# Optimization experiments

Measured on AMD Instinct MI355X. Metric: run time of the kernel, lower is better.

The kernel has to match this reference:

```python
import jax, jax.numpy as jnp
import numpy as np

K3 = 27            # kernel_size**3
PAIRS_PER_K = 131072  # pairs per kernel offset (equal-size segments)
N_VOX = 262144     # active voxels (stride-1, same grid: N_in == N_out)
C_IN = 32
C_OUT = 32


def setup_inputs() -> dict:
    key = jax.random.key(0)
    k1, k2, k3, k4 = jax.random.split(key, 4)
    M = K3 * PAIRS_PER_K
    in_feature = jax.random.normal(k1, (N_VOX, C_IN), dtype=jnp.float32)
    kernel = jax.random.normal(k2, (K3, C_IN, C_OUT), dtype=jnp.float32) * (1.0 / np.sqrt(C_IN * K3))
    bias = jax.random.normal(k3, (C_OUT,), dtype=jnp.float32) * 0.01
    # nbmap[:, 0] = input voxel index, nbmap[:, 1] = output voxel index,
    # sorted by kernel offset (offset k owns rows [k*P, (k+1)*P)).
    nbmap = jax.random.randint(k4, (M, 2), 0, N_VOX, dtype=jnp.int32)
    nbsizes = jnp.full((K3,), PAIRS_PER_K, dtype=jnp.int32)
    return {"in_feature": in_feature, "kernel": kernel, "bias": bias,
            "nbmap": nbmap, "nbsizes": nbsizes}


def reference(in_feature, kernel, bias, nbmap, nbsizes):
    """Gather -> per-offset GEMM -> scatter-add, matching
    ext.conv.sparse_convolution for a stride-1 non-transposed conv where
    nbmap rows are grouped by kernel offset with equal segment sizes."""
    k3, c_in, c_out = kernel.shape
    m = nbmap.shape[0]
    p = m // k3  # pairs per offset (static)
    n_out = in_feature.shape[0]  # same grid, stride 1
    # gather input features for every (input, output) pair  [M, C_in]
    gathered = in_feature[nbmap[:, 0]]
    # batched GEMM: one [P, C_in] x [C_in, C_out] per kernel offset
    contrib = jnp.einsum('kpi,kio->kpo', gathered.reshape(k3, p, c_in), kernel)
    contrib = contrib.reshape(m, c_out)
    # scatter-add contributions into output voxels
    out = jax.ops.segment_sum(contrib, nbmap[:, 1], num_segments=n_out)
    return out + bias
```

## Files before the change

kernel.cpp:

```cpp
#include <hip/hip_runtime.h>
#include <hip/hip_bf16.h>


#define N_VOX    262144
#define LOG2_NV  18
#define C_CH     32
#define K3       27
#define LOG2_PPK 17
#define BLOCK    256
#define FLAG_FIN 0x40000000
#define ECAP     4096
#define PLPAD    36
#define FRAGN    (K3 * 2 * 64)
#define NF16     (N_VOX * 4)

typedef __attribute__((ext_vector_type(8))) short bf16x8;
typedef __attribute__((ext_vector_type(4))) float f32x4;
typedef unsigned long long ull;

#define PMASK   0x3FFFFFull
#define EMPTY2(w) (((w) >> 58) == 0x3Full)

__device__ __forceinline__ unsigned short f2bf(float f) {
  union { __hip_bfloat16 h; unsigned short u; } cv;
  cv.h = __float2bfloat16(f);
  return cv.u;
}

__global__ __launch_bounds__(BLOCK) void setup_kernel(
    int4* __restrict__ clrT, long nt4, int4* __restrict__ clrC, long nc4,
    const float* __restrict__ in_feature, unsigned short* __restrict__ feat16,
    int use16, const float* __restrict__ kernel_w,
    unsigned short* __restrict__ Bf) {
  long idx = (long)blockIdx.x * BLOCK + threadIdx.x;
  if (idx < nt4) {
    clrT[idx] = make_int4(-1, -1, -1, -1);
    return;
  }
  idx -= nt4;
  if (idx < nc4) {
    clrC[idx] = make_int4(0, 0, 0, 0);
    return;
  }
  idx -= nc4;
  if (use16) {
    if (idx < NF16) {
      const float4* src = (const float4*)in_feature + (idx << 1);
      float4 f0 = src[0], f1 = src[1];
      union { unsigned short u[8]; uint4 v; } pk;
      pk.u[0] = f2bf(f0.x); pk.u[1] = f2bf(f0.y);
      pk.u[2] = f2bf(f0.z); pk.u[3] = f2bf(f0.w);
      pk.u[4] = f2bf(f1.x); pk.u[5] = f2bf(f1.y);
      pk.u[6] = f2bf(f1.z); pk.u[7] = f2bf(f1.w);
      ((uint4*)feat16)[idx] = pk.v;
      return;
    }
    idx -= NF16;
  }
  if (idx < FRAGN) {
    int wid = (int)idx;
    int lane = wid & 63;
    int kc = wid >> 6;
    int k = kc >> 1, t = kc & 1;
    int i0 = (lane >> 4) * 8;
    int c = t * 16 + (lane & 15);
    union { unsigned short u[8]; uint4 v; } pk;
#pragma unroll
    for (int j = 0; j < 8; ++j)
      pk.u[j] = f2bf(kernel_w[(k << 10) + (i0 + j) * C_CH + c]);
    ((uint4*)Bf)[wid] = pk.v;
  }
}

__global__ __launch_bounds__(BLOCK) void passA_packed(
    const int4* __restrict__ nbmap2, ull* __restrict__ T64, int Mq) {
  int q = blockIdx.x * BLOCK + threadIdx.x;
  if (q >= Mq) return;
  int4 na = nbmap2[q * 2];
  int4 nb = nbmap2[q * 2 + 1];
  int p0 = q << 2, p1 = p0 | 1, p2 = p0 | 2, p3 = p0 | 3;
  const ull EM = 0x3Full << 58;
  T64[((long)(p0 >> LOG2_PPK) << LOG2_NV) + na.y] =
      (ull)p0 | ((ull)na.x << 22) | EM;
  T64[((long)(p1 >> LOG2_PPK) << LOG2_NV) + na.w] =
      (ull)p1 | ((ull)na.z << 22) | EM;
  T64[((long)(p2 >> LOG2_PPK) << LOG2_NV) + nb.y] =
      (ull)p2 | ((ull)nb.x << 22) | EM;
  T64[((long)(p3 >> LOG2_PPK) << LOG2_NV) + nb.w] =
      (ull)p3 | ((ull)nb.z << 22) | EM;
}

__device__ __forceinline__ void ovf_push(
    int vox, int k, int in, int* __restrict__ ovf_cnt, int* __restrict__ ovf,
    int S2, int* __restrict__ ecnt, int2* __restrict__ elist) {
  int pos = atomicAdd(&ovf_cnt[vox], 1);
  if (pos < S2) {
    ovf[(pos << LOG2_NV) + vox] = (k << LOG2_NV) | in;
  } else {
    int ep = atomicAdd(ecnt, 1);
    if (ep < ECAP) elist[ep] = make_int2(vox, (k << LOG2_NV) | in);
  }
}

__device__ __forceinline__ void resolve_packed(
    int p, int vox, int in, ull w, ull* __restrict__ T64, long idx,
    int* __restrict__ ovf_cnt, int* __restrict__ ovf, int S2,
    int* __restrict__ ecnt, int2* __restrict__ elist) {
  if ((w & PMASK) == (ull)p) return;
  ull cur = w;
  for (;;) {
    if (!EMPTY2(cur)) break;
    ull nw = (cur & ((1ull << 40) - 1)) | ((ull)in << 40);
    ull old = atomicCAS(&T64[idx], cur, nw);
    if (old == cur) return;
    cur = old;
  }
  ovf_push(vox, p >> LOG2_PPK, in, ovf_cnt, ovf, S2, ecnt, elist);
}

__global__ __launch_bounds__(BLOCK) void passB_packed(
    const int4* __restrict__ nbmap2, ull* __restrict__ T64,
    int* __restrict__ ovf_cnt, int* __restrict__ ovf, int S2,
    int* __restrict__ ecnt, int2* __restrict__ elist, int Mq) {
  int q = blockIdx.x * BLOCK + threadIdx.x;
  if (q >= Mq) return;
  int4 na = nbmap2[q * 2];
  int4 nb = nbmap2[q * 2 + 1];
  int p0 = q << 2, p1 = p0 | 1, p2 = p0 | 2, p3 = p0 | 3;
  long i0 = ((long)(p0 >> LOG2_PPK) << LOG2_NV) + na.y;
  long i1 = ((long)(p1 >> LOG2_PPK) << LOG2_NV) + na.w;
  long i2 = ((long)(p2 >> LOG2_PPK) << LOG2_NV) + nb.y;
  long i3 = ((long)(p3 >> LOG2_PPK) << LOG2_NV) + nb.w;
  ull w0 = T64[i0];
  ull w1 = T64[i1];
  ull w2 = T64[i2];
  ull w3 = T64[i3];
  resolve_packed(p0, na.y, na.x, w0, T64, i0, ovf_cnt, ovf, S2, ecnt, elist);
  resolve_packed(p1, na.w, na.z, w1, T64, i1, ovf_cnt, ovf, S2, ecnt, elist);
  resolve_packed(p2, nb.y, nb.x, w2, T64, i2, ovf_cnt, ovf, S2, ecnt, elist);
  resolve_packed(p3, nb.w, nb.z, w3, T64, i3, ovf_cnt, ovf, S2, ecnt, elist);
}

__global__ __launch_bounds__(BLOCK) void passA_legacy(
    const int2* __restrict__ nbmap, int* __restrict__ T, int M) {
  int p = blockIdx.x * BLOCK + threadIdx.x;
  if (p >= M) return;
  int2 nb = nbmap[p];
  T[((p >> LOG2_PPK) << LOG2_NV) + nb.y] = p;
}

__global__ __launch_bounds__(BLOCK) void passB_legacy(
    const int2* __restrict__ nbmap, int* __restrict__ T,
    int* __restrict__ ovf_cnt, int* __restrict__ ovf, int S2,
    int* __restrict__ ecnt, int2* __restrict__ elist, int M) {
  int p = blockIdx.x * BLOCK + threadIdx.x;
  if (p >= M) return;
  int2 nb = nbmap[p];
  int idx = ((p >> LOG2_PPK) << LOG2_NV) + nb.y;
  if (T[idx] == p) {
    T[idx] = FLAG_FIN | nb.x;
  } else {
    ovf_push(nb.y, p >> LOG2_PPK, nb.x, ovf_cnt, ovf, S2, ecnt, elist);
  }
}

template <int PACKED, int F16>
__global__ __launch_bounds__(BLOCK, 4) void gather_splitk_kernel(
    const float* __restrict__ in_feature,
    const unsigned short* __restrict__ feat16,
    const float* __restrict__ kernel_w,
    const float* __restrict__ bias,
    const void* __restrict__ Tv,
    const int* __restrict__ ovf_cnt,
    const int* __restrict__ ovf,
    const unsigned short* __restrict__ Bf,
    float* __restrict__ out, int S2) {
  __shared__ float plane[4][16][PLPAD];
  __shared__ int flatE[256];
  __shared__ int scnt[16];

  const int tid = threadIdx.x;
  const int w = tid >> 6;
  const int lane = tid & 63;
  const int r16 = lane & 15;
  const int quad = lane >> 4;
  const int vb = blockIdx.x << 4;

  const int er = tid & 15;
  const int ej = tid >> 4;
  int eval = 0;
  if (ej < S2)
    eval = ovf[(ej << LOG2_NV) + vb + er];
  if (tid < 16) {
    int c = ovf_cnt[vb + tid];
    scnt[tid] = c < S2 ? c : S2;
  }
  const int kb = w * 7;
  const int kn = (w == 3) ? 6 : 7;
  const int v = vb + r16;

  ull wv[7];
  if (PACKED) {
    const ull* T64 = (const ull*)Tv;
#pragma unroll
    for (int d = 0; d < 7; ++d)
      wv[d] = (d < kn) ? T64[((long)(kb + d) << LOG2_NV) + v] : ~0ull;
  } else {
    const int* T = (const int*)Tv;
#pragma unroll
    for (int d = 0; d < 7; ++d) {
      int t = (d < kn) ? T[((kb + d) << LOG2_NV) + v] : -1;
      wv[d] = (t >= 0) ? (((ull)(t & 0x3FFFF) << 22) | (0x3Full << 58))
                       : ~0ull;
    }
  }
  __syncthreads();

  int myb = 0, tot = 0;
#pragma unroll
  for (int q = 0; q < 16; ++q) {
    int cq = scnt[q];
    if (q < er) myb += cq;
    tot += cq;
  }
  if (ej < scnt[er])
    flatE[myb + ej] = (er << 24) | eval;
  __syncthreads();

  bf16x8 R0[7], R1[7];
#pragma unroll
  for (int d = 0; d < 7; ++d) {
    bool val1 = (wv[d] & PMASK) != PMASK;
    int in = val1 ? (int)((wv[d] >> 22) & 0x3FFFF) : 0;
    bf16x8 a;
    if (F16) {
      a = *reinterpret_cast<const bf16x8*>(feat16 + (in << 5) + (quad << 3));
    } else {
      const float4* ap = (const float4*)(in_feature + (in << 5) + (quad << 3));
      float4 f0 = ap[0], f1 = ap[1];
      a[0] = (short)f2bf(f0.x); a[1] = (short)f2bf(f0.y);
      a[2] = (short)f2bf(f0.z); a[3] = (short)f2bf(f0.w);
      a[4] = (short)f2bf(f1.x); a[5] = (short)f2bf(f1.y);
      a[6] = (short)f2bf(f1.z); a[7] = (short)f2bf(f1.w);
    }
    if (!val1) a = (bf16x8)0;
    R0[d] = a;
  }
  if (PACKED) {
#pragma unroll
    for (int d = 0; d < 7; ++d) {
      bool val2 = !EMPTY2(wv[d]);
      int in = val2 ? (int)((wv[d] >> 40) & 0x3FFFF) : 0;
      bf16x8 a;
      if (F16) {
        a = *reinterpret_cast<const bf16x8*>(feat16 + (in << 5) + (quad << 3));
      } else {
        const float4* ap =
            (const float4*)(in_feature + (in << 5) + (quad << 3));
        float4 f0 = ap[0], f1 = ap[1];
        a[0] = (short)f2bf(f0.x); a[1] = (short)f2bf(f0.y);
        a[2] = (short)f2bf(f0.z); a[3] = (short)f2bf(f0.w);
        a[4] = (short)f2bf(f1.x); a[5] = (short)f2bf(f1.y);
        a[6] = (short)f2bf(f1.z); a[7] = (short)f2bf(f1.w);
      }
      if (!val2) a = (bf16x8)0;
      R1[d] = a;
    }
  }

  f32x4 acc0 = {0.f, 0.f, 0.f, 0.f};
  f32x4 acc1 = {0.f, 0.f, 0.f, 0.f};
  const uint4* bfp = (const uint4*)Bf;
#pragma unroll
  for (int d = 0; d < 7; ++d) {
    if (d < kn) {
      int k = kb + d;
      uint4 h0 = bfp[(k * 2 + 0) * 64 + lane];
      uint4 h1 = bfp[(k * 2 + 1) * 64 + lane];
      acc0 = __builtin_amdgcn_mfma_f32_16x16x32_bf16(
          R0[d], *reinterpret_cast<const bf16x8*>(&h0), acc0, 0, 0, 0);
      acc1 = __builtin_amdgcn_mfma_f32_16x16x32_bf16(
          R0[d], *reinterpret_cast<const bf16x8*>(&h1), acc1, 0, 0, 0);
    }
  }
  if (PACKED) {
#pragma unroll
    for (int d = 0; d < 7; ++d) {
      if (d < kn) {
        int k = kb + d;
        uint4 h0 = bfp[(k * 2 + 0) * 64 + lane];
        uint4 h1 = bfp[(k * 2 + 1) * 64 + lane];
        acc0 = __builtin_amdgcn_mfma_f32_16x16x32_bf16(
            R1[d], *reinterpret_cast<const bf16x8*>(&h0), acc0, 0, 0, 0);
        acc1 = __builtin_amdgcn_mfma_f32_16x16x32_bf16(
            R1[d], *reinterpret_cast<const bf16x8*>(&h1), acc1, 0, 0, 0);
      }
    }
  }

#pragma unroll
  for (int reg = 0; reg < 4; ++reg) {
    int row = quad * 4 + reg;
    plane[w][row][r16] = acc0[reg];
    plane[w][row][16 + r16] = acc1[reg];
  }

  const int c32 = lane & 31, h = lane >> 5;
  int i = w;
  int e_cur = 0;
  float4 p0, p1, p2, p3;
  if (i < tot) {
    e_cur = flatE[i];
    const float4* ar =
        (const float4*)(in_feature + ((e_cur & 0x3FFFF) << 5) + (h << 4));
    p0 = ar[0]; p1 = ar[1]; p2 = ar[2]; p3 = ar[3];
  }
  while (i < tot) {
    const int e = e_cur;
    float4 q0 = p0, q1 = p1, q2 = p2, q3 = p3;
    const int inext = i + 4;
    if (inext < tot) {
      e_cur = flatE[inext];
      const float4* ar =
          (const float4*)(in_feature + ((e_cur & 0x3FFFF) << 5) + (h << 4));
      p0 = ar[0]; p1 = ar[1]; p2 = ar[2]; p3 = ar[3];
    }
    const int k2 = (e >> LOG2_NV) & 31;
    const int rr = (e >> 24) & 15;
    const float* wcol = kernel_w + (k2 << 10) + (h << 4) * C_CH + c32;
    float psum = 0.f;
    psum = fmaf(q0.x, wcol[0 * C_CH], psum);
    psum = fmaf(q0.y, wcol[1 * C_CH], psum);
    psum = fmaf(q0.z, wcol[2 * C_CH], psum);
    psum = fmaf(q0.w, wcol[3 * C_CH], psum);
    psum = fmaf(q1.x, wcol[4 * C_CH], psum);
    psum = fmaf(q1.y, wcol[5 * C_CH], psum);
    psum = fmaf(q1.z, wcol[6 * C_CH], psum);
    psum = fmaf(q1.w, wcol[7 * C_CH], psum);
    psum = fmaf(q2.x, wcol[8 * C_CH], psum);
    psum = fmaf(q2.y, wcol[9 * C_CH], psum);
    psum = fmaf(q2.z, wcol[10 * C_CH], psum);
    psum = fmaf(q2.w, wcol[11 * C_CH], psum);
    psum = fmaf(q3.x, wcol[12 * C_CH], psum);
    psum = fmaf(q3.y, wcol[13 * C_CH], psum);
    psum = fmaf(q3.z, wcol[14 * C_CH], psum);
    psum = fmaf(q3.w, wcol[15 * C_CH], psum);
    psum += __shfl_xor(psum, 32);
    if (h == 0) plane[w][rr][c32] += psum;
    i = inext;
  }

  __syncthreads();
  const int mr = tid >> 4;
  const int mc = (tid & 15) << 1;
  float s0 = plane[0][mr][mc] + plane[1][mr][mc] + plane[2][mr][mc] +
             plane[3][mr][mc] + bias[mc];
  float s1 = plane[0][mr][mc + 1] + plane[1][mr][mc + 1] +
             plane[2][mr][mc + 1] + plane[3][mr][mc + 1] + bias[mc + 1];
  float2 o; o.x = s0; o.y = s1;
  *(float2*)(out + ((vb + mr) << 5) + mc) = o;
}

__global__ __launch_bounds__(BLOCK) void emergency_kernel(
    const float* __restrict__ in_feature, const float* __restrict__ kernel_w,
    const int* __restrict__ ecnt, const int2* __restrict__ elist,
    float* __restrict__ out) {
  int e = blockIdx.x * BLOCK + threadIdx.x;
  int n = *ecnt;
  if (n > ECAP) n = ECAP;
  if (e >= n) return;
  int2 ent = elist[e];
  int v = ent.x, k = ent.y >> LOG2_NV, in = ent.y & 0x3FFFF;
  float a[C_CH];
  const float4* ar = (const float4*)(in_feature + (in << 5));
#pragma unroll
  for (int q = 0; q < 8; ++q) ((float4*)a)[q] = ar[q];
  for (int c = 0; c < C_CH; ++c) {
    float s = 0.f;
#pragma unroll
    for (int i = 0; i < C_CH; ++i)
      s = fmaf(a[i], kernel_w[(k << 10) + i * C_CH + c], s);
    atomicAdd(&out[v * C_CH + c], s);
  }
}

__global__ __launch_bounds__(BLOCK) void init_bias_kernel(
    float* __restrict__ out, const float* __restrict__ bias, int n4) {
  int idx = blockIdx.x * blockDim.x + threadIdx.x;
  if (idx >= n4) return;
  ((float4*)out)[idx] = ((const float4*)bias)[idx & 7];
}

__global__ __launch_bounds__(BLOCK) void scatter_conv_kernel(
    const float* __restrict__ in_feature, const float* __restrict__ kernel_w,
    const int* __restrict__ nbmap, float* __restrict__ out) {
  const int k = blockIdx.x >> 9;
  const int pair = blockIdx.x * BLOCK + threadIdx.x;
  const float* __restrict__ Wk = kernel_w + k * (C_CH * C_CH);
  const int2 nb = ((const int2*)nbmap)[pair];
  const float4* __restrict__ inrow =
      (const float4*)(in_feature + (long)nb.x * C_CH);
  float a[C_CH];
#pragma unroll
  for (int j = 0; j < 8; ++j) ((float4*)a)[j] = inrow[j];
  float acc[C_CH];
#pragma unroll
  for (int c = 0; c < C_CH; ++c) acc[c] = 0.0f;
#pragma unroll
  for (int i = 0; i < C_CH; ++i) {
    const float av = a[i];
#pragma unroll
    for (int c = 0; c < C_CH; ++c)
      acc[c] = fmaf(av, Wk[i * C_CH + c], acc[c]);
  }
  float* __restrict__ orow = out + (long)nb.y * C_CH;
#pragma unroll
  for (int c = 0; c < C_CH; ++c) atomicAdd(orow + c, acc[c]);
}

extern "C" void kernel_launch(void* const* d_in, const int* in_sizes, int n_in,
                              void* d_out, int out_size, void* d_ws,
                              size_t ws_size, hipStream_t stream) {
  const float* in_feature = (const float*)d_in[0];
  const float* kernel_w   = (const float*)d_in[1];
  const float* bias       = (const float*)d_in[2];
  const int*   nbmap      = (const int*)d_in[3];
  float* out = (float*)d_out;
  const int M = in_sizes[3] / 2;
  const int Mq = M / 4;

  const long FIXED = 64 + 2 * ECAP + 13824;
  long ws_ints = (long)(ws_size / 4);
  long planes = (ws_ints - FIXED) / N_VOX;
  int packed = 0, use16 = 0;
  long s2c;
  if (planes >= 75) {
    packed = 1; use16 = 1;
    s2c = planes - 71;
    if (s2c > 7) s2c = 7;
  } else if (planes >= 59) {
    packed = 1;
    s2c = planes - 55;
    if (s2c > 7) s2c = 7;
  } else {
    s2c = planes - 28;
    if (s2c > 15) s2c = 15;
  }
  int S2 = (int)s2c;

  if (!packed && S2 < 4) {
    const int n4 = out_size / 4;
    init_bias_kernel<<<(n4 + BLOCK - 1) / BLOCK, BLOCK, 0, stream>>>(out, bias,
                                                                     n4);
    scatter_conv_kernel<<<M / BLOCK, BLOCK, 0, stream>>>(in_feature, kernel_w,
                                                         nbmap, out);
    return;
  }

  const long planesT = packed ? 2L * K3 : (long)K3;
  int* Tbase    = (int*)d_ws;
  int* ovf_cnt  = Tbase + planesT * N_VOX;
  int* ecnt     = ovf_cnt + N_VOX;
  int2* elist   = (int2*)(ecnt + 64);
  unsigned short* Bf = (unsigned short*)(ecnt + 64 + 2 * ECAP);
  int* ovf      = ((int*)Bf) + 13824;
  unsigned short* feat16 = (unsigned short*)(ovf + (long)S2 * N_VOX);

  const long nt4 = planesT * N_VOX / 4;
  const long nc4 = (N_VOX + 64) / 4;
  const long total = nt4 + nc4 + (use16 ? (long)NF16 : 0) + FRAGN;
  const long sblocks = (total + BLOCK - 1) / BLOCK;
  setup_kernel<<<(int)sblocks, BLOCK, 0, stream>>>(
      (int4*)Tbase, nt4, (int4*)ovf_cnt, nc4, in_feature, feat16, use16,
      kernel_w, Bf);

  if (packed) {
    passA_packed<<<(Mq + BLOCK - 1) / BLOCK, BLOCK, 0, stream>>>(
        (const int4*)nbmap, (ull*)Tbase, Mq);
    passB_packed<<<(Mq + BLOCK - 1) / BLOCK, BLOCK, 0, stream>>>(
        (const int4*)nbmap, (ull*)Tbase, ovf_cnt, ovf, S2, ecnt, elist, Mq);
    if (use16)
      gather_splitk_kernel<1, 1><<<N_VOX / 16, BLOCK, 0, stream>>>(
          in_feature, feat16, kernel_w, bias, (const void*)Tbase, ovf_cnt,
          ovf, Bf, out, S2);
    else
      gather_splitk_kernel<1, 0><<<N_VOX / 16, BLOCK, 0, stream>>>(
          in_feature, feat16, kernel_w, bias, (const void*)Tbase, ovf_cnt,
          ovf, Bf, out, S2);
  } else {
    passA_legacy<<<(M + BLOCK - 1) / BLOCK, BLOCK, 0, stream>>>(
        (const int2*)nbmap, Tbase, M);
    passB_legacy<<<(M + BLOCK - 1) / BLOCK, BLOCK, 0, stream>>>(
        (const int2*)nbmap, Tbase, ovf_cnt, ovf, S2, ecnt, elist, M);
    gather_splitk_kernel<0, 0><<<N_VOX / 16, BLOCK, 0, stream>>>(
        in_feature, feat16, kernel_w, bias, (const void*)Tbase, ovf_cnt, ovf,
        Bf, out, S2);
  }
  emergency_kernel<<<ECAP / BLOCK, BLOCK, 0, stream>>>(in_feature, kernel_w,
                                                       ecnt, elist, out);
}
```

Before: 362.0 us.

## Replace two-pass write/resolve table build with single atomicMax claim pass

The two kernels that built the packed 64-bit per-(offset, voxel) table, a plain-store pass followed by a CAS resolve pass, are merged into one kernel. Each pair now does a 64-bit atomicMax with a key that puts the pair index in the high bits, then resolves losers into a second-slot CAS or the overflow list. The table word layout is redesigned (zero means empty, bit 0 flags the second input), and the setup fill value and the gather kernel's decoding change to match. This removes one full pass over nbmap and the table, at the cost of atomic RMW traffic on every insert.

```diff
diff --git a/kernel.cpp b/kernel.cpp
--- a/kernel.cpp
+++ b/kernel.cpp
@@ -18,9 +18,6 @@
 typedef __attribute__((ext_vector_type(4))) float f32x4;
 typedef unsigned long long ull;
 
-#define PMASK   0x3FFFFFull
-#define EMPTY2(w) (((w) >> 58) == 0x3Full)
-
 __device__ __forceinline__ unsigned short f2bf(float f) {
   union { __hip_bfloat16 h; unsigned short u; } cv;
   cv.h = __float2bfloat16(f);
@@ -28,13 +25,13 @@
 }
 
 __global__ __launch_bounds__(BLOCK) void setup_kernel(
-    int4* __restrict__ clrT, long nt4, int4* __restrict__ clrC, long nc4,
-    const float* __restrict__ in_feature, unsigned short* __restrict__ feat16,
-    int use16, const float* __restrict__ kernel_w,
-    unsigned short* __restrict__ Bf) {
+    int4* __restrict__ clrT, long nt4, int cv, int4* __restrict__ clrC,
+    long nc4, const float* __restrict__ in_feature,
+    unsigned short* __restrict__ feat16, int use16,
+    const float* __restrict__ kernel_w, unsigned short* __restrict__ Bf) {
   long idx = (long)blockIdx.x * BLOCK + threadIdx.x;
   if (idx < nt4) {
-    clrT[idx] = make_int4(-1, -1, -1, -1);
+    clrT[idx] = make_int4(cv, cv, cv, cv);
     return;
   }
   idx -= nt4;
@@ -72,24 +69,6 @@
   }
 }
 
-__global__ __launch_bounds__(BLOCK) void passA_packed(
-    const int4* __restrict__ nbmap2, ull* __restrict__ T64, int Mq) {
-  int q = blockIdx.x * BLOCK + threadIdx.x;
-  if (q >= Mq) return;
-  int4 na = nbmap2[q * 2];
-  int4 nb = nbmap2[q * 2 + 1];
-  int p0 = q << 2, p1 = p0 | 1, p2 = p0 | 2, p3 = p0 | 3;
-  const ull EM = 0x3Full << 58;
-  T64[((long)(p0 >> LOG2_PPK) << LOG2_NV) + na.y] =
-      (ull)p0 | ((ull)na.x << 22) | EM;
-  T64[((long)(p1 >> LOG2_PPK) << LOG2_NV) + na.w] =
-      (ull)p1 | ((ull)na.z << 22) | EM;
-  T64[((long)(p2 >> LOG2_PPK) << LOG2_NV) + nb.y] =
-      (ull)p2 | ((ull)nb.x << 22) | EM;
-  T64[((long)(p3 >> LOG2_PPK) << LOG2_NV) + nb.w] =
-      (ull)p3 | ((ull)nb.z << 22) | EM;
-}
-
 __device__ __forceinline__ void ovf_push(
     int vox, int k, int in, int* __restrict__ ovf_cnt, int* __restrict__ ovf,
     int S2, int* __restrict__ ecnt, int2* __restrict__ elist) {
@@ -102,23 +81,40 @@
   }
 }
 
-__device__ __forceinline__ void resolve_packed(
-    int p, int vox, int in, ull w, ull* __restrict__ T64, long idx,
+__device__ __forceinline__ void in2_insert(
+    ull* __restrict__ T64, long idx, ull cur, int vox, int k, int in,
     int* __restrict__ ovf_cnt, int* __restrict__ ovf, int S2,
     int* __restrict__ ecnt, int2* __restrict__ elist) {
-  if ((w & PMASK) == (ull)p) return;
-  ull cur = w;
   for (;;) {
-    if (!EMPTY2(cur)) break;
-    ull nw = (cur & ((1ull << 40) - 1)) | ((ull)in << 40);
-    ull old = atomicCAS(&T64[idx], cur, nw);
-    if (old == cur) return;
-    cur = old;
-  }
-  ovf_push(vox, p >> LOG2_PPK, in, ovf_cnt, ovf, S2, ecnt, elist);
-}
-
-__global__ __launch_bounds__(BLOCK) void passB_packed(
+    if (cur & 1ull) {
+      ovf_push(vox, k, in, ovf_cnt, ovf, S2, ecnt, elist);
+      return;
+    }
+    ull nw = cur | ((ull)in << 6) | 1ull;
+    ull got = atomicCAS(&T64[idx], cur, nw);
+    if (got == cur) return;
+    cur = got;
+  }
+}
+
+__device__ __forceinline__ void resolve_max(
+    ull* __restrict__ T64, long idx, ull myw, ull old, int vox, int k, int in,
+    int* __restrict__ ovf_cnt, int* __restrict__ ovf, int S2,
+    int* __restrict__ ecnt, int2* __restrict__ elist) {
+  if (old == 0) return;
+  if (old < myw) {
+    int in1p = (int)((old >> 24) & 0x3FFFF);
+    if (old & 1ull) {
+      int in2p = (int)((old >> 6) & 0x3FFFF);
+      ovf_push(vox, k, in2p, ovf_cnt, ovf, S2, ecnt, elist);
+    }
+    in2_insert(T64, idx, myw, vox, k, in1p, ovf_cnt, ovf, S2, ecnt, elist);
+  } else {
+    in2_insert(T64, idx, old, vox, k, in, ovf_cnt, ovf, S2, ecnt, elist);
+  }
+}
+
+__global__ __launch_bounds__(BLOCK) void claim_max_kernel(
     const int4* __restrict__ nbmap2, ull* __restrict__ T64,
     int* __restrict__ ovf_cnt, int* __restrict__ ovf, int S2,
     int* __restrict__ ecnt, int2* __restrict__ elist, int Mq) {
@@ -127,18 +123,24 @@
   int4 na = nbmap2[q * 2];
   int4 nb = nbmap2[q * 2 + 1];
   int p0 = q << 2, p1 = p0 | 1, p2 = p0 | 2, p3 = p0 | 3;
-  long i0 = ((long)(p0 >> LOG2_PPK) << LOG2_NV) + na.y;
-  long i1 = ((long)(p1 >> LOG2_PPK) << LOG2_NV) + na.w;
-  long i2 = ((long)(p2 >> LOG2_PPK) << LOG2_NV) + nb.y;
-  long i3 = ((long)(p3 >> LOG2_PPK) << LOG2_NV) + nb.w;
-  ull w0 = T64[i0];
-  ull w1 = T64[i1];
-  ull w2 = T64[i2];
-  ull w3 = T64[i3];
-  resolve_packed(p0, na.y, na.x, w0, T64, i0, ovf_cnt, ovf, S2, ecnt, elist);
-  resolve_packed(p1, na.w, na.z, w1, T64, i1, ovf_cnt, ovf, S2, ecnt, elist);
-  resolve_packed(p2, nb.y, nb.x, w2, T64, i2, ovf_cnt, ovf, S2, ecnt, elist);
-  resolve_packed(p3, nb.w, nb.z, w3, T64, i3, ovf_cnt, ovf, S2, ecnt, elist);
+  int k0 = p0 >> LOG2_PPK, k1 = p1 >> LOG2_PPK;
+  int k2 = p2 >> LOG2_PPK, k3 = p3 >> LOG2_PPK;
+  long i0 = ((long)k0 << LOG2_NV) + na.y;
+  long i1 = ((long)k1 << LOG2_NV) + na.w;
+  long i2 = ((long)k2 << LOG2_NV) + nb.y;
+  long i3 = ((long)k3 << LOG2_NV) + nb.w;
+  ull w0 = ((ull)(p0 + 1) << 42) | ((ull)na.x << 24);
+  ull w1 = ((ull)(p1 + 1) << 42) | ((ull)na.z << 24);
+  ull w2 = ((ull)(p2 + 1) << 42) | ((ull)nb.x << 24);
+  ull w3 = ((ull)(p3 + 1) << 42) | ((ull)nb.z << 24);
+  ull o0 = atomicMax(&T64[i0], w0);
+  ull o1 = atomicMax(&T64[i1], w1);
+  ull o2 = atomicMax(&T64[i2], w2);
+  ull o3 = atomicMax(&T64[i3], w3);
+  resolve_max(T64, i0, w0, o0, na.y, k0, na.x, ovf_cnt, ovf, S2, ecnt, elist);
+  resolve_max(T64, i1, w1, o1, na.w, k1, na.z, ovf_cnt, ovf, S2, ecnt, elist);
+  resolve_max(T64, i2, w2, o2, nb.y, k2, nb.x, ovf_cnt, ovf, S2, ecnt, elist);
+  resolve_max(T64, i3, w3, o3, nb.w, k3, nb.z, ovf_cnt, ovf, S2, ecnt, elist);
 }
 
 __global__ __launch_bounds__(BLOCK) void passA_legacy(
@@ -204,14 +206,13 @@
     const ull* T64 = (const ull*)Tv;
 #pragma unroll
     for (int d = 0; d < 7; ++d)
-      wv[d] = (d < kn) ? T64[((long)(kb + d) << LOG2_NV) + v] : ~0ull;
+      wv[d] = (d < kn) ? T64[((long)(kb + d) << LOG2_NV) + v] : 0ull;
   } else {
     const int* T = (const int*)Tv;
 #pragma unroll
     for (int d = 0; d < 7; ++d) {
       int t = (d < kn) ? T[((kb + d) << LOG2_NV) + v] : -1;
-      wv[d] = (t >= 0) ? (((ull)(t & 0x3FFFF) << 22) | (0x3Full << 58))
-                       : ~0ull;
+      wv[d] = (t >= 0) ? ((1ull << 42) | ((ull)(t & 0x3FFFF) << 24)) : 0ull;
     }
   }
   __syncthreads();
@@ -230,8 +231,8 @@
   bf16x8 R0[7], R1[7];
 #pragma unroll
   for (int d = 0; d < 7; ++d) {
-    bool val1 = (wv[d] & PMASK) != PMASK;
-    int in = val1 ? (int)((wv[d] >> 22) & 0x3FFFF) : 0;
+    bool val1 = (wv[d] >> 42) != 0;
+    int in = val1 ? (int)((wv[d] >> 24) & 0x3FFFF) : 0;
     bf16x8 a;
     if (F16) {
       a = *reinterpret_cast<const bf16x8*>(feat16 + (in << 5) + (quad << 3));
@@ -249,8 +250,8 @@
   if (PACKED) {
 #pragma unroll
     for (int d = 0; d < 7; ++d) {
-      bool val2 = !EMPTY2(wv[d]);
-      int in = val2 ? (int)((wv[d] >> 40) & 0x3FFFF) : 0;
+      bool val2 = (wv[d] & 1ull) != 0;
+      int in = val2 ? (int)((wv[d] >> 6) & 0x3FFFF) : 0;
       bf16x8 a;
       if (F16) {
         a = *reinterpret_cast<const bf16x8*>(feat16 + (in << 5) + (quad << 3));
@@ -471,13 +472,11 @@
   const long total = nt4 + nc4 + (use16 ? (long)NF16 : 0) + FRAGN;
   const long sblocks = (total + BLOCK - 1) / BLOCK;
   setup_kernel<<<(int)sblocks, BLOCK, 0, stream>>>(
-      (int4*)Tbase, nt4, (int4*)ovf_cnt, nc4, in_feature, feat16, use16,
-      kernel_w, Bf);
+      (int4*)Tbase, nt4, packed ? 0 : -1, (int4*)ovf_cnt, nc4, in_feature,
+      feat16, use16, kernel_w, Bf);
 
   if (packed) {
-    passA_packed<<<(Mq + BLOCK - 1) / BLOCK, BLOCK, 0, stream>>>(
-        (const int4*)nbmap, (ull*)Tbase, Mq);
-    passB_packed<<<(Mq + BLOCK - 1) / BLOCK, BLOCK, 0, stream>>>(
+    claim_max_kernel<<<(Mq + BLOCK - 1) / BLOCK, BLOCK, 0, stream>>>(
         (const int4*)nbmap, (ull*)Tbase, ovf_cnt, ovf, S2, ecnt, elist, Mq);
     if (use16)
       gather_splitk_kernel<1, 1><<<N_VOX / 16, BLOCK, 0, stream>>>(
```

Measured after the change: 416.2 us. +15.0%, slower.

## Fuse setup and claim passes into one cooperative kernel with grid syncs

Applied to the files above, without the earlier changes.

Replaces the separate setup, passA and passB launches with a single cooperative kernel of fixed grid size that clears tables, converts features and weights, writes claims, then resolves collisions, separated by grid-wide barriers. The emergency overflow handling moves into the tail of the gather kernel, where each block scans the overflow list for its own voxels. This removes several kernel launches and the inter-kernel gaps, but it depends on cooperative launch, hardcodes the problem size, and makes every gather block scan the overflow list.

```diff
diff --git a/kernel.cpp b/kernel.cpp
--- a/kernel.cpp
+++ b/kernel.cpp
@@ -1,5 +1,8 @@
 #include <hip/hip_runtime.h>
 #include <hip/hip_bf16.h>
+#include <hip/hip_cooperative_groups.h>
+
+namespace cg = cooperative_groups;
 
 
 #define N_VOX    262144
@@ -13,6 +16,7 @@
 #define PLPAD    36
 #define FRAGN    (K3 * 2 * 64)
 #define NF16     (N_VOX * 4)
+#define CBLOCKS  864
 
 typedef __attribute__((ext_vector_type(8))) short bf16x8;
 typedef __attribute__((ext_vector_type(4))) float f32x4;
@@ -27,14 +31,131 @@
   return cv.u;
 }
 
-__global__ __launch_bounds__(BLOCK) void setup_kernel(
-    int4* __restrict__ clrT, long nt4, int4* __restrict__ clrC, long nc4,
+__device__ __forceinline__ void ovf_push(
+    int vox, int k, int in, int* __restrict__ ovf_cnt, int* __restrict__ ovf,
+    int S2, int* __restrict__ ecnt, int2* __restrict__ elist) {
+  int pos = atomicAdd(&ovf_cnt[vox], 1);
+  if (pos < S2) {
+    ovf[(pos << LOG2_NV) + vox] = (k << LOG2_NV) | in;
+  } else {
+    int ep = atomicAdd(ecnt, 1);
+    if (ep < ECAP) elist[ep] = make_int2(vox, (k << LOG2_NV) | in);
+  }
+}
+
+__device__ __forceinline__ void resolve_packed(
+    int p, int vox, int in, ull w, ull* __restrict__ T64, long idx,
+    int* __restrict__ ovf_cnt, int* __restrict__ ovf, int S2,
+    int* __restrict__ ecnt, int2* __restrict__ elist) {
+  if ((w & PMASK) == (ull)p) return;
+  ull cur = w;
+  for (;;) {
+    if (!EMPTY2(cur)) break;
+    ull nw = (cur & ((1ull << 40) - 1)) | ((ull)in << 40);
+    ull old = atomicCAS(&T64[idx], cur, nw);
+    if (old == cur) return;
+    cur = old;
+  }
+  ovf_push(vox, p >> LOG2_PPK, in, ovf_cnt, ovf, S2, ecnt, elist);
+}
+
+__device__ __forceinline__ void feat16_item(
+    const float* __restrict__ in_feature, unsigned short* __restrict__ feat16,
+    long idx) {
+  const float4* src = (const float4*)in_feature + (idx << 1);
+  float4 f0 = src[0], f1 = src[1];
+  union { unsigned short u[8]; uint4 v; } pk;
+  pk.u[0] = f2bf(f0.x); pk.u[1] = f2bf(f0.y);
+  pk.u[2] = f2bf(f0.z); pk.u[3] = f2bf(f0.w);
+  pk.u[4] = f2bf(f1.x); pk.u[5] = f2bf(f1.y);
+  pk.u[6] = f2bf(f1.z); pk.u[7] = f2bf(f1.w);
+  ((uint4*)feat16)[idx] = pk.v;
+}
+
+__device__ __forceinline__ void bf_item(
+    const float* __restrict__ kernel_w, unsigned short* __restrict__ Bf,
+    int wid) {
+  int lane = wid & 63;
+  int kc = wid >> 6;
+  int k = kc >> 1, t = kc & 1;
+  int i0 = (lane >> 4) * 8;
+  int c = t * 16 + (lane & 15);
+  union { unsigned short u[8]; uint4 v; } pk;
+#pragma unroll
+  for (int j = 0; j < 8; ++j)
+    pk.u[j] = f2bf(kernel_w[(k << 10) + (i0 + j) * C_CH + c]);
+  ((uint4*)Bf)[wid] = pk.v;
+}
+
+__global__ __launch_bounds__(BLOCK, 4) void fused_setup_claim(
+    const int4* __restrict__ nbmap2, ull* __restrict__ T64,
+    int* __restrict__ ovf_cnt, int* __restrict__ ovf, int S2,
+    int* __restrict__ ecnt, int2* __restrict__ elist,
     const float* __restrict__ in_feature, unsigned short* __restrict__ feat16,
     int use16, const float* __restrict__ kernel_w,
     unsigned short* __restrict__ Bf) {
+  const int t = blockIdx.x * BLOCK + threadIdx.x;
+  const long NT = (long)CBLOCKS * BLOCK;
+
+  {
+    int4* clrT = (int4*)T64;
+    const int4 m1 = make_int4(-1, -1, -1, -1);
+#pragma unroll
+    for (int i = 0; i < 16; ++i) clrT[(long)i * NT + t] = m1;
+    if (t < (N_VOX + 64) / 4) ((int4*)ovf_cnt)[t] = make_int4(0, 0, 0, 0);
+    if (use16)
+      for (long i = t; i < NF16; i += NT) feat16_item(in_feature, feat16, i);
+    if (t < FRAGN) bf_item(kernel_w, Bf, t);
+  }
+  cg::this_grid().sync();
+
+  {
+    const ull EM = 0x3Full << 58;
+#pragma unroll
+    for (int j = 0; j < 8; ++j) {
+      int4 A = nbmap2[(long)8 * t + j];
+      int pa = (t << 4) | (j << 1);
+      int pb = pa | 1;
+      T64[((long)(pa >> LOG2_PPK) << LOG2_NV) + A.y] =
+          (ull)pa | ((ull)A.x << 22) | EM;
+      T64[((long)(pb >> LOG2_PPK) << LOG2_NV) + A.w] =
+          (ull)pb | ((ull)A.z << 22) | EM;
+    }
+  }
+  cg::this_grid().sync();
+
+#pragma unroll 1
+  for (int g = 3; g >= 0; --g) {
+    int4 A = nbmap2[(long)8 * t + 2 * g];
+    int4 B = nbmap2[(long)8 * t + 2 * g + 1];
+    int pa = (t << 4) | (g << 2);
+    long i0 = ((long)((pa + 0) >> LOG2_PPK) << LOG2_NV) + A.y;
+    long i1 = ((long)((pa + 1) >> LOG2_PPK) << LOG2_NV) + A.w;
+    long i2 = ((long)((pa + 2) >> LOG2_PPK) << LOG2_NV) + B.y;
+    long i3 = ((long)((pa + 3) >> LOG2_PPK) << LOG2_NV) + B.w;
+    ull w0 = T64[i0];
+    ull w1 = T64[i1];
+    ull w2 = T64[i2];
+    ull w3 = T64[i3];
+    resolve_packed(pa + 0, A.y, A.x, w0, T64, i0, ovf_cnt, ovf, S2, ecnt,
+                   elist);
+    resolve_packed(pa + 1, A.w, A.z, w1, T64, i1, ovf_cnt, ovf, S2, ecnt,
+                   elist);
+    resolve_packed(pa + 2, B.y, B.x, w2, T64, i2, ovf_cnt, ovf, S2, ecnt,
+                   elist);
+    resolve_packed(pa + 3, B.w, B.z, w3, T64, i3, ovf_cnt, ovf, S2, ecnt,
+                   elist);
+  }
+}
+
+__global__ __launch_bounds__(BLOCK) void setup_kernel(
+    int4* __restrict__ clrT, long nt4, int cv, int4* __restrict__ clrC,
+    long nc4, const float* __restrict__ in_feature,
+    unsigned short* __restrict__ feat16, int use16,
+    const float* __restrict__ kernel_w, unsigned short* __restrict__ Bf) {
   long idx = (long)blockIdx.x * BLOCK + threadIdx.x;
   if (idx < nt4) {
-    clrT[idx] = make_int4(-1, -1, -1, -1);
+    clrT[idx] = make_int4(cv, cv, cv, cv);
     return;
   }
   idx -= nt4;
@@ -45,31 +166,12 @@
   idx -= nc4;
   if (use16) {
     if (idx < NF16) {
-      const float4* src = (const float4*)in_feature + (idx << 1);
-      float4 f0 = src[0], f1 = src[1];
-      union { unsigned short u[8]; uint4 v; } pk;
-      pk.u[0] = f2bf(f0.x); pk.u[1] = f2bf(f0.y);
-      pk.u[2] = f2bf(f0.z); pk.u[3] = f2bf(f0.w);
-      pk.u[4] = f2bf(f1.x); pk.u[5] = f2bf(f1.y);
-      pk.u[6] = f2bf(f1.z); pk.u[7] = f2bf(f1.w);
-      ((uint4*)feat16)[idx] = pk.v;
+      feat16_item(in_feature, feat16, idx);
       return;
     }
     idx -= NF16;
   }
-  if (idx < FRAGN) {
-    int wid = (int)idx;
-    int lane = wid & 63;
-    int kc = wid >> 6;
-    int k = kc >> 1, t = kc & 1;
-    int i0 = (lane >> 4) * 8;
-    int c = t * 16 + (lane & 15);
-    union { unsigned short u[8]; uint4 v; } pk;
-#pragma unroll
-    for (int j = 0; j < 8; ++j)
-      pk.u[j] = f2bf(kernel_w[(k << 10) + (i0 + j) * C_CH + c]);
-    ((uint4*)Bf)[wid] = pk.v;
-  }
+  if (idx < FRAGN) bf_item(kernel_w, Bf, (int)idx);
 }
 
 __global__ __launch_bounds__(BLOCK) void passA_packed(
@@ -88,34 +190,6 @@
       (ull)p2 | ((ull)nb.x << 22) | EM;
   T64[((long)(p3 >> LOG2_PPK) << LOG2_NV) + nb.w] =
       (ull)p3 | ((ull)nb.z << 22) | EM;
-}
-
-__device__ __forceinline__ void ovf_push(
-    int vox, int k, int in, int* __restrict__ ovf_cnt, int* __restrict__ ovf,
-    int S2, int* __restrict__ ecnt, int2* __restrict__ elist) {
-  int pos = atomicAdd(&ovf_cnt[vox], 1);
-  if (pos < S2) {
-    ovf[(pos << LOG2_NV) + vox] = (k << LOG2_NV) | in;
-  } else {
-    int ep = atomicAdd(ecnt, 1);
-    if (ep < ECAP) elist[ep] = make_int2(vox, (k << LOG2_NV) | in);
-  }
-}
-
-__device__ __forceinline__ void resolve_packed(
-    int p, int vox, int in, ull w, ull* __restrict__ T64, long idx,
-    int* __restrict__ ovf_cnt, int* __restrict__ ovf, int S2,
-    int* __restrict__ ecnt, int2* __restrict__ elist) {
-  if ((w & PMASK) == (ull)p) return;
-  ull cur = w;
-  for (;;) {
-    if (!EMPTY2(cur)) break;
-    ull nw = (cur & ((1ull << 40) - 1)) | ((ull)in << 40);
-    ull old = atomicCAS(&T64[idx], cur, nw);
-    if (old == cur) return;
-    cur = old;
-  }
-  ovf_push(vox, p >> LOG2_PPK, in, ovf_cnt, ovf, S2, ecnt, elist);
 }
 
 __global__ __launch_bounds__(BLOCK) void passB_packed(
@@ -173,6 +247,8 @@
     const void* __restrict__ Tv,
     const int* __restrict__ ovf_cnt,
     const int* __restrict__ ovf,
+    const int* __restrict__ ecnt,
+    const int2* __restrict__ elist,
     const unsigned short* __restrict__ Bf,
     float* __restrict__ out, int S2) {
   __shared__ float plane[4][16][PLPAD];
@@ -359,28 +435,23 @@
              plane[2][mr][mc + 1] + plane[3][mr][mc + 1] + bias[mc + 1];
   float2 o; o.x = s0; o.y = s1;
   *(float2*)(out + ((vb + mr) << 5) + mc) = o;
-}
-
-__global__ __launch_bounds__(BLOCK) void emergency_kernel(
-    const float* __restrict__ in_feature, const float* __restrict__ kernel_w,
-    const int* __restrict__ ecnt, const int2* __restrict__ elist,
-    float* __restrict__ out) {
-  int e = blockIdx.x * BLOCK + threadIdx.x;
-  int n = *ecnt;
-  if (n > ECAP) n = ECAP;
-  if (e >= n) return;
-  int2 ent = elist[e];
-  int v = ent.x, k = ent.y >> LOG2_NV, in = ent.y & 0x3FFFF;
-  float a[C_CH];
-  const float4* ar = (const float4*)(in_feature + (in << 5));
-#pragma unroll
-  for (int q = 0; q < 8; ++q) ((float4*)a)[q] = ar[q];
-  for (int c = 0; c < C_CH; ++c) {
-    float s = 0.f;
-#pragma unroll
-    for (int i = 0; i < C_CH; ++i)
-      s = fmaf(a[i], kernel_w[(k << 10) + i * C_CH + c], s);
-    atomicAdd(&out[v * C_CH + c], s);
+
+  __syncthreads();
+  int ne = *ecnt;
+  if (ne > ECAP) ne = ECAP;
+  for (int ei = (tid >> 5); ei < ne; ei += 8) {
+    int2 ent = elist[ei];
+    unsigned dv = (unsigned)(ent.x - vb);
+    if (dv < 16u) {
+      int kk = ent.y >> LOG2_NV, in = ent.y & 0x3FFFF;
+      int c = tid & 31;
+      const float* arow = in_feature + (in << 5);
+      const float* wcol = kernel_w + (kk << 10) + c;
+      float s = 0.f;
+#pragma unroll
+      for (int ii = 0; ii < C_CH; ++ii) s = fmaf(arow[ii], wcol[ii * C_CH], s);
+      atomicAdd(&out[((long)ent.x << 5) + c], s);
+    }
   }
 }
 
@@ -466,36 +537,52 @@
   int* ovf      = ((int*)Bf) + 13824;
   unsigned short* feat16 = (unsigned short*)(ovf + (long)S2 * N_VOX);
 
-  const long nt4 = planesT * N_VOX / 4;
-  const long nc4 = (N_VOX + 64) / 4;
-  const long total = nt4 + nc4 + (use16 ? (long)NF16 : 0) + FRAGN;
-  const long sblocks = (total + BLOCK - 1) / BLOCK;
-  setup_kernel<<<(int)sblocks, BLOCK, 0, stream>>>(
-      (int4*)Tbase, nt4, (int4*)ovf_cnt, nc4, in_feature, feat16, use16,
-      kernel_w, Bf);
+  int coop_done = 0;
+  if (packed && M == 3538944) {
+    const int4* nb4 = (const int4*)nbmap;
+    ull* T64p = (ull*)Tbase;
+    void* cargs[] = {(void*)&nb4,       (void*)&T64p,    (void*)&ovf_cnt,
+                     (void*)&ovf,       (void*)&S2,      (void*)&ecnt,
+                     (void*)&elist,     (void*)&in_feature,
+                     (void*)&feat16,    (void*)&use16,   (void*)&kernel_w,
+                     (void*)&Bf};
+    hipError_t cerr = hipLaunchCooperativeKernel(
+        fused_setup_claim, dim3(CBLOCKS), dim3(BLOCK), cargs, 0u, stream);
+    if (cerr == hipSuccess) coop_done = 1;
+  }
+  if (!coop_done) {
+    const long nt4 = planesT * N_VOX / 4;
+    const long nc4 = (N_VOX + 64) / 4;
+    const long total = nt4 + nc4 + (use16 ? (long)NF16 : 0) + FRAGN;
+    const long sblocks = (total + BLOCK - 1) / BLOCK;
+    setup_kernel<<<(int)sblocks, BLOCK, 0, stream>>>(
+        (int4*)Tbase, nt4, -1, (int4*)ovf_cnt, nc4, in_feature, feat16,
+        use16, kernel_w, Bf);
+    if (packed) {
+      passA_packed<<<(Mq + BLOCK - 1) / BLOCK, BLOCK, 0, stream>>>(
+          (const int4*)nbmap, (ull*)Tbase, Mq);
+      passB_packed<<<(Mq + BLOCK - 1) / BLOCK, BLOCK, 0, stream>>>(
+          (const int4*)nbmap, (ull*)Tbase, ovf_cnt, ovf, S2, ecnt, elist, Mq);
+    } else {
+      passA_legacy<<<(M + BLOCK - 1) / BLOCK, BLOCK, 0, stream>>>(
+          (const int2*)nbmap, Tbase, M);
+      passB_legacy<<<(M + BLOCK - 1) / BLOCK, BLOCK, 0, stream>>>(
+          (const int2*)nbmap, Tbase, ovf_cnt, ovf, S2, ecnt, elist, M);
+    }
+  }
 
   if (packed) {
-    passA_packed<<<(Mq + BLOCK - 1) / BLOCK, BLOCK, 0, stream>>>(
-        (const int4*)nbmap, (ull*)Tbase, Mq);
-    passB_packed<<<(Mq + BLOCK - 1) / BLOCK, BLOCK, 0, stream>>>(
-        (const int4*)nbmap, (ull*)Tbase, ovf_cnt, ovf, S2, ecnt, elist, Mq);
     if (use16)
       gather_splitk_kernel<1, 1><<<N_VOX / 16, BLOCK, 0, stream>>>(
           in_feature, feat16, kernel_w, bias, (const void*)Tbase, ovf_cnt,
-          ovf, Bf, out, S2);
+          ovf, ecnt, elist, Bf, out, S2);
     else
       gather_splitk_kernel<1, 0><<<N_VOX / 16, BLOCK, 0, stream>>>(
           in_feature, feat16, kernel_w, bias, (const void*)Tbase, ovf_cnt,
-          ovf, Bf, out, S2);
+          ovf, ecnt, elist, Bf, out, S2);
   } else {
-    passA_legacy<<<(M + BLOCK - 1) / BLOCK, BLOCK, 0, stream>>>(
-        (const int2*)nbmap, Tbase, M);
-    passB_legacy<<<(M + BLOCK - 1) / BLOCK, BLOCK, 0, stream>>>(
-        (const int2*)nbmap, Tbase, ovf_cnt, ovf, S2, ecnt, elist, M);
     gather_splitk_kernel<0, 0><<<N_VOX / 16, BLOCK, 0, stream>>>(
         in_feature, feat16, kernel_w, bias, (const void*)Tbase, ovf_cnt, ovf,
-        Bf, out, S2);
-  }
-  emergency_kernel<<<ECAP / BLOCK, BLOCK, 0, stream>>>(in_feature, kernel_w,
-                                                       ecnt, elist, out);
-}
+        ecnt, elist, Bf, out, S2);
+  }
+}
```

Measured after the change: 631.4 us. +74.4%, slower.
